# Optimization experiments

Measured on AMD Instinct MI355X. Metric: run time of the kernel, lower is better.

## Reference

```python
import jax, jax.numpy as jnp
import numpy as np

N = 50000      # nodes
E = 400000     # edges
D_IN = 128; D_HID = 128; D_OUT = 128
C = 8          # n_channel (== channel_dim)
CNF = 8        # channel_nf
DIM = 3        # spatial dim
EPS = 1e-3     # module eps
BN_EPS = 1e-5


def _pool_matrix(n_channel):
    # RollerPooling: pool_matrix[i] averages a sliding upper-triangular window of size (n-i)
    ones = np.ones((n_channel, n_channel), dtype=np.float32)
    mats = []
    for i in range(n_channel):
        w = n_channel - i
        mats.append((np.triu(ones) - np.triu(ones, k=w)) / w)
    return jnp.asarray(np.stack(mats))  # [C, C, C]


def setup_inputs() -> dict:
    key = jax.random.key(0)
    ks = jax.random.split(key, 20)
    s = 0.02
    src = jax.random.randint(ks[0], (E,), 0, N)
    tgt = jax.random.randint(ks[1], (E,), 0, N)
    rel = jnp.zeros((E,), dtype=src.dtype)  # num_relation = 1
    edge_list = jnp.stack([src, tgt, rel], axis=1)
    inp = {
        "h": jax.random.normal(ks[2], (N, D_IN), jnp.float32),
        "coords": jax.random.normal(ks[3], (N, C, DIM), jnp.float32),
        "channel_attr": jax.random.normal(ks[4], (N, C, CNF), jnp.float32),
        "channel_weights": jax.random.randint(ks[5], (N, C), 0, 3).astype(jnp.float32),
        "edge_weights": jax.random.uniform(ks[6], (E,), jnp.float32),
        "edge_list": edge_list,
        # parameters
        "rl_w": jax.random.normal(ks[7], (CNF * CNF, CNF), jnp.float32) * s,
        "rl_b": jnp.zeros((CNF,), jnp.float32),
        "m_w1": jax.random.normal(ks[8], (2 * D_IN + CNF, D_HID), jnp.float32) * s,
        "m_b1": jnp.zeros((D_HID,), jnp.float32),
        "m_w2": jax.random.normal(ks[9], (D_HID, D_HID), jnp.float32) * s,
        "m_b2": jnp.zeros((D_HID,), jnp.float32),
        "c_w1": jax.random.normal(ks[10], (D_HID, D_HID), jnp.float32) * s,
        "c_b1": jnp.zeros((D_HID,), jnp.float32),
        "c_w2": jax.random.normal(ks[11], (D_HID, C), jnp.float32) * 0.001,  # xavier gain=0.001
        "het_w": jax.random.normal(ks[12], (D_HID, D_OUT), jnp.float32) * s,
        "het_b": jnp.zeros((D_OUT,), jnp.float32),
        "bn_gamma": jnp.ones((D_OUT,), jnp.float32),
        "bn_beta": jnp.zeros((D_OUT,), jnp.float32),
        "w_r": jnp.ones((1,), jnp.float32),
    }
    return inp


def reference(h, coords, channel_attr, channel_weights, edge_weights,
              rl_w, rl_b, m_w1, m_b1, m_w2, m_b2, c_w1, c_b1, c_w2,
              het_w, het_b, bn_gamma, bn_beta, w_r, edge_list):
    silu = jax.nn.silu
    src, tgt, rel = edge_list[:, 0], edge_list[:, 1], edge_list[:, 2]
    n_channel = coords.shape[1]
    num_nodes = h.shape[0]

    # --- radial feature ---
    # pairwise channel distances per edge: [E, C, C]
    diff = coords[tgt][:, :, None, :] - coords[src][:, None, :, :]
    coord_msg = jnp.linalg.norm(diff, axis=-1)
    coord_msg = coord_msg / (jnp.max(coord_msg) + EPS)
    cw = channel_weights
    coord_msg = coord_msg * (cw[tgt][:, :, None] * cw[src][:, None, :])
    # attr_t^T @ msg @ attr_s -> [E, CNF, CNF]
    radial = jnp.einsum('eca,ecd,edb->eab', channel_attr[tgt], coord_msg, channel_attr[src])
    radial = radial.reshape(radial.shape[0], -1)
    radial = radial / (jnp.linalg.norm(radial, axis=-1, keepdims=True) + EPS)
    radial = radial @ rl_w + rl_b  # [E, CNF]

    mask = (cw != 0)
    csum = mask.sum(-1)  # [N]
    pooled_col = (coords[src] * mask[src][:, :, None].astype(coords.dtype)).sum(1)
    pooled_col = pooled_col / (csum[src][:, None].astype(coords.dtype) + EPS)
    coord_diff = coords[tgt] - pooled_col[:, None, :]  # [E, C, DIM]

    # --- message MLP (dropout = identity in eval) ---
    x = jnp.concatenate([h[tgt], h[src], radial], axis=-1)
    m = silu(x @ m_w1 + m_b1)
    m = silu(m @ m_w2 + m_b2)  # [E, hidden]

    # --- coord message with RollerPooling ---
    edge_feat = silu(m @ c_w1 + c_b1) @ c_w2  # [E, C]
    pm = _pool_matrix(n_channel)
    ts = jnp.clip(csum[tgt] - 1, 0, n_channel - 1)
    pooled_edge = jnp.einsum('eij,ej->ei', pm[ts], edge_feat)[..., None]  # [E, C, 1]
    coord_message = coord_diff * pooled_edge  # [E, C, DIM]

    # --- aggregate (scatter to target nodes) ---
    ew = edge_weights[:, None]
    node_agg = jax.ops.segment_sum(m * ew, tgt, num_segments=num_nodes)  # [N, hidden]
    wcm = w_r[rel][:, None, None] * coord_message
    coord_sum = jax.ops.segment_sum(wcm, tgt, num_segments=num_nodes)
    cnt = jax.ops.segment_sum(jnp.ones((wcm.shape[0],), wcm.dtype), tgt, num_segments=num_nodes)
    coord_agg = coord_sum / jnp.clip(cnt, 1.0)[:, None, None]  # mean aggregation

    # --- combine ---
    out = node_agg @ het_w + het_b
    # BatchNorm1d in eval mode with default running stats (mean=0, var=1)
    out = out / jnp.sqrt(1.0 + BN_EPS) * bn_gamma + bn_beta
    out = silu(out)
    node_output = h + out
    coord_output = coords + coord_agg
    return node_output, coord_output
```

## Files before the change

kernel.cpp:

```cpp
#include <hip/hip_runtime.h>

#define NN 50000
#define NE 400000
#define D 128
#define MST 136
#define EPSV 1e-3f

typedef unsigned short u16;
typedef unsigned int u32;
typedef __attribute__((ext_vector_type(4))) float f32x4;
typedef __attribute__((ext_vector_type(4))) float float4v;
typedef __attribute__((ext_vector_type(8))) short short8;
typedef __attribute__((ext_vector_type(8))) unsigned short ushort8;
typedef __attribute__((ext_vector_type(4))) unsigned short ushort4v;

__device__ __forceinline__ u16 f2b(float f){
  u32 u = __float_as_uint(f);
  u32 r = u + 0x7fffu + ((u >> 16) & 1u);
  return (u16)(r >> 16);
}
__device__ __forceinline__ float b2f(u16 s){ return __uint_as_float(((u32)s) << 16); }
__device__ __forceinline__ float silu_f(float x){
  return x * __builtin_amdgcn_rcpf(1.f + __expf(-x));
}
__device__ __forceinline__ void atomAddF(float* p, float v){ unsafeAtomicAdd(p, v); }

__global__ void k_prep_h(const float* __restrict__ h, u16* __restrict__ hbf){
  int i = (blockIdx.x * 256 + threadIdx.x) * 4;
  if (i < NN * D){
    float4v v = *(const float4v*)(h + i);
    ushort4v o = { f2b(v[0]), f2b(v[1]), f2b(v[2]), f2b(v[3]) };
    *(ushort4v*)(hbf + i) = o;
  }
}

__global__ void k_prep_w(const float* __restrict__ m_w1, const float* __restrict__ m_b1,
                         const float* __restrict__ m_w2, const float* __restrict__ c_w1,
                         const float* __restrict__ c_w2, const float* __restrict__ het_w,
                         u16* __restrict__ W12t, u16* __restrict__ W1cT,
                         u16* __restrict__ W2t, u16* __restrict__ C1t,
                         u16* __restrict__ HtT, u16* __restrict__ C2t){
  int i = blockIdx.x * 256 + threadIdx.x;
  if (i < 256 * 128){
    int c = i >> 7, k = i & 127;
    W12t[i] = f2b(c < 128 ? m_w1[k * D + c] : m_w1[(128 + k) * D + (c - 128)]);
    return;
  }
  i -= 256 * 128;
  if (i < 128 * 32){
    int c = i >> 5, j = i & 31;
    W1cT[i] = (j < 8) ? f2b(m_w1[(256 + j) * D + c]) : (j == 8 ? f2b(m_b1[c]) : (u16)0);
    return;
  }
  i -= 128 * 32;
  if (i < D * D){ int c = i >> 7, k = i & 127; W2t[i] = f2b(m_w2[k * D + c]); return; }
  i -= D * D;
  if (i < D * D){ int c = i >> 7, k = i & 127; C1t[i] = f2b(c_w1[k * D + c]); return; }
  i -= D * D;
  if (i < D * D){ int c = i >> 7, k = i & 127; HtT[i] = f2b(het_w[k * D + c]); return; }
  i -= D * D;
  if (i < 16 * D){ int n = i >> 7, k = i & 127; C2t[i] = f2b(n < 8 ? c_w2[k * 8 + n] : 0.f); return; }
}

__global__ void k_node_pre(const float* __restrict__ coords, const float* __restrict__ cw,
                           float* __restrict__ pooled, int* __restrict__ tsn){
  int n = blockIdx.x * 256 + threadIdx.x;
  if (n >= NN) return;
  int cs = 0; float px = 0.f, py = 0.f, pz = 0.f;
  #pragma unroll
  for (int c = 0; c < 8; c++){
    float w = cw[n * 8 + c];
    if (w != 0.f){
      cs++;
      px += coords[(size_t)n * 24 + c * 3 + 0];
      py += coords[(size_t)n * 24 + c * 3 + 1];
      pz += coords[(size_t)n * 24 + c * 3 + 2];
    }
  }
  float inv = 1.f / ((float)cs + EPSV);
  pooled[n * 3 + 0] = px * inv;
  pooled[n * 3 + 1] = py * inv;
  pooled[n * 3 + 2] = pz * inv;
  int ts = cs - 1; ts = ts < 0 ? 0 : (ts > 7 ? 7 : ts);
  tsn[n] = ts;
}

__global__ __launch_bounds__(256) void k_edge_max(const float* __restrict__ coords,
                                                  const int* __restrict__ el,
                                                  u32* __restrict__ maxsq, u32* __restrict__ cnt){
  int e = blockIdx.x * 256 + threadIdx.x;
  float vm = 0.f;
  if (e < NE){
    int s = el[e * 3 + 0], t = el[e * 3 + 1];
    float ct[24], cs_[24];
    const float4v* pt = (const float4v*)(coords + (size_t)t * 24);
    const float4v* ps = (const float4v*)(coords + (size_t)s * 24);
    #pragma unroll
    for (int i = 0; i < 6; i++){
      float4v v = pt[i];
      ct[i*4] = v[0]; ct[i*4+1] = v[1]; ct[i*4+2] = v[2]; ct[i*4+3] = v[3];
    }
    #pragma unroll
    for (int i = 0; i < 6; i++){
      float4v v = ps[i];
      cs_[i*4] = v[0]; cs_[i*4+1] = v[1]; cs_[i*4+2] = v[2]; cs_[i*4+3] = v[3];
    }
    #pragma unroll
    for (int c1 = 0; c1 < 8; c1++){
      #pragma unroll
      for (int c2 = 0; c2 < 8; c2++){
        float dx = ct[c1*3+0] - cs_[c2*3+0];
        float dy = ct[c1*3+1] - cs_[c2*3+1];
        float dz = ct[c1*3+2] - cs_[c2*3+2];
        vm = fmaxf(vm, dx*dx + dy*dy + dz*dz);
      }
    }
    atomicAdd(&cnt[t], 1u);
  }
  __shared__ float red[256];
  red[threadIdx.x] = vm;
  __syncthreads();
  for (int s2 = 128; s2 > 0; s2 >>= 1){
    if (threadIdx.x < s2) red[threadIdx.x] = fmaxf(red[threadIdx.x], red[threadIdx.x + s2]);
    __syncthreads();
  }
  if (threadIdx.x == 0) atomicMax(maxsq, __float_as_uint(red[0]));
}

__global__ __launch_bounds__(1024) void k_scan(const u32* __restrict__ cnt,
                                               u32* __restrict__ row_start,
                                               u32* __restrict__ fill_ptr){
  __shared__ u32 s[1024];
  const int tid = threadIdx.x;
  const int base = tid * 49;
  u32 tot = 0;
  #pragma unroll 1
  for (int k = 0; k < 49; k++){
    int i = base + k;
    if (i < NN) tot += cnt[i];
  }
  s[tid] = tot;
  __syncthreads();
  for (int off = 1; off < 1024; off <<= 1){
    u32 v = (tid >= off) ? s[tid - off] : 0u;
    __syncthreads();
    s[tid] += v;
    __syncthreads();
  }
  u32 running = s[tid] - tot;
  #pragma unroll 1
  for (int k = 0; k < 49; k++){
    int i = base + k;
    if (i <= NN){
      row_start[i] = running;
      if (i < NN){ fill_ptr[i] = running; running += cnt[i]; }
    }
  }
}

__global__ __launch_bounds__(256) void k_fill(const int* __restrict__ el,
                                              u32* __restrict__ fill_ptr,
                                              int* __restrict__ eidx){
  int e = blockIdx.x * 256 + threadIdx.x;
  if (e >= NE) return;
  int t = el[e * 3 + 1];
  u32 pos = atomicAdd(&fill_ptr[t], 1u);
  eidx[pos] = e;
}

__global__ __launch_bounds__(256) void k_radial(const float* __restrict__ coords,
                                                const float* __restrict__ attr,
                                                const float* __restrict__ cw,
                                                const int* __restrict__ el,
                                                const int* __restrict__ eidx,
                                                const float* __restrict__ ewg,
                                                const float* __restrict__ rl_w,
                                                const float* __restrict__ rl_b,
                                                const u32* __restrict__ maxsq,
                                                u16* __restrict__ rad8b,
                                                u32* __restrict__ st_s,
                                                float* __restrict__ ew_s){
  __shared__ float sct[64][24], scs[64][24], sAs[64][64], scwt[64][8], scws[64][8], stmp[64][64];
  const int tid = threadIdx.x;
  const int er = tid >> 2;
  const int q = tid & 3;
  const int p = blockIdx.x * 64 + er;
  const int e = eidx[p];
  const int s = el[e * 3 + 0];
  const int t = el[e * 3 + 1];
  if (q == 0){
    st_s[p] = ((u32)t << 16) | (u32)s;
    ew_s[p] = ewg[e];
  }

  #pragma unroll
  for (int i = 0; i < 6; i++) sct[er][q * 6 + i] = coords[(size_t)t * 24 + q * 6 + i];
  #pragma unroll
  for (int i = 0; i < 6; i++) scs[er][q * 6 + i] = coords[(size_t)s * 24 + q * 6 + i];
  #pragma unroll
  for (int i = 0; i < 16; i++) sAs[er][q * 16 + i] = attr[(size_t)s * 64 + q * 16 + i];
  #pragma unroll
  for (int i = 0; i < 2; i++){
    scwt[er][q * 2 + i] = cw[(size_t)t * 8 + q * 2 + i];
    scws[er][q * 2 + i] = cw[(size_t)s * 8 + q * 2 + i];
  }
  __syncthreads();

  const float scale = 1.f / (sqrtf(__uint_as_float(*maxsq)) + EPSV);

  float tmp[2][8];
  #pragma unroll
  for (int ci = 0; ci < 2; ci++)
    #pragma unroll
    for (int b = 0; b < 8; b++) tmp[ci][b] = 0.f;
  #pragma unroll
  for (int d = 0; d < 8; d++){
    float asd[8];
    #pragma unroll
    for (int b = 0; b < 8; b++) asd[b] = sAs[er][d * 8 + b];
    #pragma unroll
    for (int ci = 0; ci < 2; ci++){
      int c = q * 2 + ci;
      float dx = sct[er][c * 3 + 0] - scs[er][d * 3 + 0];
      float dy = sct[er][c * 3 + 1] - scs[er][d * 3 + 1];
      float dz = sct[er][c * 3 + 2] - scs[er][d * 3 + 2];
      float msg = sqrtf(dx * dx + dy * dy + dz * dz) * scale * scwt[er][c] * scws[er][d];
      #pragma unroll
      for (int b = 0; b < 8; b++) tmp[ci][b] += msg * asd[b];
    }
  }
  #pragma unroll
  for (int ci = 0; ci < 2; ci++)
    #pragma unroll
    for (int b = 0; b < 8; b++) stmp[er][(q * 2 + ci) * 8 + b] = tmp[ci][b];
  __syncthreads();

  float rad[2][8];
  #pragma unroll
  for (int ai = 0; ai < 2; ai++)
    #pragma unroll
    for (int b = 0; b < 8; b++) rad[ai][b] = 0.f;
  #pragma unroll
  for (int c = 0; c < 8; c++){
    float at0 = attr[(size_t)t * 64 + c * 8 + 2 * q + 0];
    float at1 = attr[(size_t)t * 64 + c * 8 + 2 * q + 1];
    #pragma unroll
    for (int b = 0; b < 8; b++){
      float tv = stmp[er][c * 8 + b];
      rad[0][b] += at0 * tv;
      rad[1][b] += at1 * tv;
    }
  }
  float sq = 0.f;
  #pragma unroll
  for (int ai = 0; ai < 2; ai++)
    #pragma unroll
    for (int b = 0; b < 8; b++) sq += rad[ai][b] * rad[ai][b];
  sq += __shfl_xor(sq, 1);
  sq += __shfl_xor(sq, 2);
  const float rn = 1.f / (sqrtf(sq) + EPSV);

  float o[8];
  #pragma unroll
  for (int j = 0; j < 8; j++) o[j] = 0.f;
  #pragma unroll
  for (int ai = 0; ai < 2; ai++){
    #pragma unroll
    for (int b = 0; b < 8; b++){
      float v = rad[ai][b] * rn;
      int row = (2 * q + ai) * 8 + b;
      #pragma unroll
      for (int j = 0; j < 8; j++) o[j] += v * rl_w[row * 8 + j];
    }
  }
  #pragma unroll
  for (int j = 0; j < 8; j++){
    o[j] += __shfl_xor(o[j], 1);
    o[j] += __shfl_xor(o[j], 2);
  }
  if (q == 0){
    ushort8 o8;
    #pragma unroll
    for (int j = 0; j < 8; j++) o8[j] = f2b(o[j] + rl_b[j]);
    *(ushort8*)(rad8b + (size_t)p * 8) = o8;
  }
}

__global__ __launch_bounds__(256) void k_hw12(const u16* __restrict__ hbf,
                                              const u16* __restrict__ W12t,
                                              float* __restrict__ hW12){
  __shared__ u16 sa[64 * MST];
  const int tid = threadIdx.x, lane = tid & 63, wv = tid >> 6, wrow = wv * 16;
  const int nb0 = blockIdx.x * 64;
  const int lc = lane & 15, lk = (lane >> 4) * 8;
  const f32x4 zero = {0.f, 0.f, 0.f, 0.f};

  #pragma unroll
  for (int jj = 0; jj < 4; jj++){
    const int flat = jj * 64 + lane;
    const int r = wrow + (flat >> 4);
    const int c8 = flat & 15;
    int rn = nb0 + r; if (rn >= NN) rn = NN - 1;
    *(ushort8*)(sa + r * MST + c8 * 8) = *(const ushort8*)(hbf + (size_t)rn * D + c8 * 8);
  }

  f32x4 acc[16];
  #pragma unroll
  for (int nb = 0; nb < 16; nb++) acc[nb] = zero;
  #pragma unroll
  for (int kb = 0; kb < 4; kb++){
    short8 a = *(const short8*)(sa + (wrow + lc) * MST + kb * 32 + lk);
    #pragma unroll
    for (int nb = 0; nb < 16; nb++){
      short8 b = *(const short8*)(W12t + (size_t)(nb * 16 + lc) * D + kb * 32 + lk);
      acc[nb] = __builtin_amdgcn_mfma_f32_16x16x32_bf16(a, b, acc[nb], 0, 0, 0);
    }
  }
  #pragma unroll
  for (int nb = 0; nb < 16; nb++){
    const int col = nb * 16 + lc;
    #pragma unroll
    for (int j = 0; j < 4; j++){
      const int row = wrow + (lane >> 4) * 4 + j;
      const int node = nb0 + row;
      if (node < NN) hW12[(size_t)node * 256 + col] = acc[nb][j];
    }
  }
}

__global__ __launch_bounds__(256, 2) void k_edge_mlp(
    const u16* __restrict__ rad8b, const u32* __restrict__ st_s,
    const float* __restrict__ ew_s, const float* __restrict__ hW12,
    const u16* __restrict__ W1cT, const u16* __restrict__ W2t,
    const u16* __restrict__ C1t, const u16* __restrict__ C2t,
    const float* __restrict__ m_b2, const float* __restrict__ c_b1,
    const int* __restrict__ tsn,
    float* __restrict__ out_node, float* __restrict__ pe8)
{
  __shared__ u16 sm[128 * MST];
  __shared__ float sef[128 * 8];
  __shared__ int s_tgt[128];
  __shared__ float s_ew[128];

  const int tid = threadIdx.x;
  const int lane = tid & 63;
  const int wv = tid >> 6;
  const int wr = wv * 32;
  const int e0 = blockIdx.x * 128;
  const int lc = lane & 15;
  const int khi = lane >> 4;
  const int lk = khi * 8;
  const f32x4 zero4 = {0.f, 0.f, 0.f, 0.f};
  const short8 zero8 = {0, 0, 0, 0, 0, 0, 0, 0};

  if (lane < 32){
    u32 v = st_s[e0 + wr + lane];
    s_tgt[wr + lane] = (int)(v >> 16);
    s_ew[wr + lane] = ew_s[e0 + wr + lane];
  }

  {
    const int r = wr + (lane >> 1);
    const int ch = (lane & 1) * 64;
    u32 v = st_s[e0 + r];
    const int t = (int)(v >> 16), s = (int)(v & 0xffffu);
    const float* pa = hW12 + (size_t)t * 256 + ch;
    const float* pb = hW12 + (size_t)s * 256 + 128 + ch;
    #pragma unroll
    for (int i = 0; i < 16; i++){
      float4v va = *(const float4v*)(pa + i * 4);
      float4v vb = *(const float4v*)(pb + i * 4);
      ushort4v o = { f2b(va[0] + vb[0]), f2b(va[1] + vb[1]),
                     f2b(va[2] + vb[2]), f2b(va[3] + vb[3]) };
      *(ushort4v*)(sm + r * MST + ch + i * 4) = o;
    }
  }

  f32x4 acc0[8], acc1[8];

  {
    short8 ar0, ar1;
    if (khi == 0){
      ar0 = *(const short8*)(rad8b + (size_t)(e0 + wr + lc) * 8);
      ar1 = *(const short8*)(rad8b + (size_t)(e0 + wr + 16 + lc) * 8);
    } else if (khi == 1){
      ar0 = zero8; ar0[0] = (short)0x3F80;
      ar1 = ar0;
    } else {
      ar0 = zero8; ar1 = zero8;
    }
    #pragma unroll
    for (int nb = 0; nb < 8; nb++){
      short8 b = *(const short8*)(W1cT + (size_t)(nb * 16 + lc) * 32 + lk);
      acc0[nb] = __builtin_amdgcn_mfma_f32_16x16x32_bf16(ar0, b, zero4, 0, 0, 0);
      acc1[nb] = __builtin_amdgcn_mfma_f32_16x16x32_bf16(ar1, b, zero4, 0, 0, 0);
    }
  }
  #pragma unroll
  for (int nb = 0; nb < 8; nb++){
    const int col = nb * 16 + lc;
    #pragma unroll
    for (int j = 0; j < 4; j++){
      const int r0 = wr + khi * 4 + j;
      const int r1 = r0 + 16;
      float v0 = silu_f(acc0[nb][j] + b2f(sm[r0 * MST + col]));
      float v1 = silu_f(acc1[nb][j] + b2f(sm[r1 * MST + col]));
      sm[r0 * MST + col] = f2b(v0);
// ... 81 lines not shown
      short8 a1 = *(const short8*)(sm + (wr + 16 + lc) * MST + kb * 32 + lk);
      short8 b = *(const short8*)(C2t + (size_t)lc * D + kb * 32 + lk);
      e40 = __builtin_amdgcn_mfma_f32_16x16x32_bf16(a0, b, e40, 0, 0, 0);
      e41 = __builtin_amdgcn_mfma_f32_16x16x32_bf16(a1, b, e41, 0, 0, 0);
    }
    if (lc < 8){
      #pragma unroll
      for (int j = 0; j < 4; j++){
        sef[(wr + khi * 4 + j) * 8 + lc] = e40[j];
        sef[(wr + 16 + khi * 4 + j) * 8 + lc] = e41[j];
      }
    }
  }

  {
    const int er = wr + (lane >> 1);
    const int q4 = (lane & 1) * 4;
    const int t = s_tgt[er];
    const int w8 = 8 - tsn[t];
    const float invw = 1.f / (float)w8;
    float4v o;
    #pragma unroll
    for (int ci = 0; ci < 4; ci++){
      const int c = q4 + ci;
      float pe = 0.f;
      const int hi = (c + w8 < 8) ? (c + w8) : 8;
      for (int j = c; j < hi; j++) pe += sef[er * 8 + j];
      o[ci] = pe * invw;
    }
    *(float4v*)(pe8 + (size_t)(e0 + er) * 8 + q4) = o;
  }
}

__global__ __launch_bounds__(256) void k_agg(
    const u32* __restrict__ row_start, const float* __restrict__ pe8,
    const u32* __restrict__ st_s, const float* __restrict__ pooled,
    const float* __restrict__ coords, const float* __restrict__ w_r,
    float* __restrict__ out_coord)
{
  const int lane = threadIdx.x & 63;
  const int wv = threadIdx.x >> 6;
  const int n = blockIdx.x * 4 + wv;
  if (n >= NN) return;
  const u32 r0 = row_start[n], r1 = row_start[n + 1];
  const int cA = lane / 3, dA = lane - cA * 3;
  float sp = 0.f, sqd = 0.f;
  for (u32 p = r0; p < r1; p++){
    if (lane < 8)  sp  += pe8[(size_t)p * 8 + lane];
    if (lane < 24) sqd += pooled[(size_t)(st_s[p] & 0xffffu) * 3 + dA] * pe8[(size_t)p * 8 + cA];
  }
  if (lane < 24){
    const float wr0 = w_r[0];
    const float spc = __shfl(sp, cA);
    const float cv = coords[(size_t)n * 24 + lane];
    const u32 deg = r1 - r0;
    const float dv = (float)(deg > 0u ? deg : 1u);
    out_coord[(size_t)n * 24 + lane] = cv + wr0 * (cv * spc - sqd) / dv;
  }
}

__global__ __launch_bounds__(256) void k_final(
    const float* __restrict__ h, const u16* __restrict__ HtT,
    const float* __restrict__ het_b, const float* __restrict__ bn_g,
    const float* __restrict__ bn_b, float* __restrict__ out_node)
{
  __shared__ u16 sa[64 * MST];
  const int tid = threadIdx.x, lane = tid & 63, wv = tid >> 6, wrow = wv * 16;
  const int nb0 = blockIdx.x * 64;
  const int lc = lane & 15, lk = (lane >> 4) * 8;
  const f32x4 zero = {0.f, 0.f, 0.f, 0.f};

  #pragma unroll
  for (int jj = 0; jj < 8; jj++){
    const int idx = jj * 64 + lane;
    const int r = wrow + (idx >> 5);
    const int c4 = (idx & 31) * 4;
    int rn = nb0 + r; if (rn >= NN) rn = NN - 1;
    float4v v = *(const float4v*)(out_node + (size_t)rn * D + c4);
    ushort4v o = { f2b(v[0]), f2b(v[1]), f2b(v[2]), f2b(v[3]) };
    *(ushort4v*)(sa + r * MST + c4) = o;
  }

  f32x4 acc[8];
  #pragma unroll
  for (int nb = 0; nb < 8; nb++) acc[nb] = zero;
  #pragma unroll
  for (int kb = 0; kb < 4; kb++){
    short8 a = *(const short8*)(sa + (wrow + lc) * MST + kb * 32 + lk);
    #pragma unroll
    for (int nb = 0; nb < 8; nb++){
      short8 b = *(const short8*)(HtT + (size_t)(nb * 16 + lc) * D + kb * 32 + lk);
      acc[nb] = __builtin_amdgcn_mfma_f32_16x16x32_bf16(a, b, acc[nb], 0, 0, 0);
    }
  }
  const float invs = rsqrtf(1.f + 1e-5f);
  #pragma unroll
  for (int nb = 0; nb < 8; nb++){
    const int col = nb * 16 + lc;
    const float hb = het_b[col], g = bn_g[col], be = bn_b[col];
    #pragma unroll
    for (int j = 0; j < 4; j++){
      const int row = wrow + (lane >> 4) * 4 + j;
      const int node = nb0 + row;
      if (node < NN){
        float v = silu_f((acc[nb][j] + hb) * invs * g + be);
        out_node[(size_t)node * D + col] = v + h[(size_t)node * D + col];
      }
    }
  }
}

extern "C" void kernel_launch(void* const* d_in, const int* in_sizes, int n_in,
                              void* d_out, int out_size, void* d_ws, size_t ws_size,
                              hipStream_t stream)
{
  const float* h      = (const float*)d_in[0];
  const float* coords = (const float*)d_in[1];
  const float* cattr  = (const float*)d_in[2];
  const float* cw     = (const float*)d_in[3];
  const float* ewg    = (const float*)d_in[4];
  const int*   el     = (const int*)  d_in[5];
  const float* rl_w   = (const float*)d_in[6];
  const float* rl_b   = (const float*)d_in[7];
  const float* m_w1   = (const float*)d_in[8];
  const float* m_b1   = (const float*)d_in[9];
  const float* m_w2   = (const float*)d_in[10];
  const float* m_b2   = (const float*)d_in[11];
  const float* c_w1   = (const float*)d_in[12];
  const float* c_b1   = (const float*)d_in[13];
  const float* c_w2   = (const float*)d_in[14];
  const float* het_w  = (const float*)d_in[15];
  const float* het_b  = (const float*)d_in[16];
  const float* bn_g   = (const float*)d_in[17];
  const float* bn_b   = (const float*)d_in[18];
  const float* w_r    = (const float*)d_in[19];

  char* wsb = (char*)d_ws;
  size_t off = 0;
  auto take = [&](size_t bytes)->char*{
    char* p = wsb + off;
    off = (off + bytes + 255) & ~(size_t)255;
    return p;
  };
  u32*   maxsq  = (u32*)  take(4);
  float* pooled = (float*)take((size_t)NN * 3 * 4);
  int*   tsn    = (int*)  take((size_t)NN * 4);
  u32*   cnt    = (u32*)  take((size_t)NN * 4);
  u16*   hbf    = (u16*)  take((size_t)NN * D * 2);
  u16*   W12t   = (u16*)  take((size_t)256 * D * 2);
  u16*   W1cT   = (u16*)  take((size_t)D * 32 * 2);
  u16*   W2t    = (u16*)  take((size_t)D * D * 2);
  u16*   C1t    = (u16*)  take((size_t)D * D * 2);
  u16*   HtT    = (u16*)  take((size_t)D * D * 2);
  u16*   C2t    = (u16*)  take((size_t)16 * D * 2);
  u32*   row_start = (u32*)  take((size_t)(NN + 1) * 4);
  u32*   fill_ptr  = (u32*)  take((size_t)NN * 4);
  int*   eidx      = (int*)  take((size_t)NE * 4);
  u32*   st_s      = (u32*)  take((size_t)NE * 4);
  float* ew_s      = (float*)take((size_t)NE * 4);
  u16*   rad8b     = (u16*)  take((size_t)NE * 8 * 2);
  float* pe8       = (float*)take((size_t)NE * 8 * 4);
  float* hW12      = (float*)take((size_t)NN * 256 * 4);
  (void)ws_size;

  float* out_node  = (float*)d_out;
  float* out_coord = out_node + (size_t)NN * D;

  (void)hipMemsetAsync(maxsq, 0, 4, stream);
  (void)hipMemsetAsync(cnt, 0, (size_t)NN * 4, stream);
  (void)hipMemsetAsync(out_node, 0, (size_t)NN * D * 4, stream);

  k_prep_h  <<<dim3((NN * D / 4 + 255) / 256), dim3(256), 0, stream>>>(h, hbf);
  k_prep_w  <<<dim3((256*128 + 128*32 + 3*D*D + 16*D + 255) / 256), dim3(256), 0, stream>>>(
        m_w1, m_b1, m_w2, c_w1, c_w2, het_w, W12t, W1cT, W2t, C1t, HtT, C2t);
  k_node_pre<<<dim3((NN + 255) / 256), dim3(256), 0, stream>>>(coords, cw, pooled, tsn);
  k_edge_max<<<dim3((NE + 255) / 256), dim3(256), 0, stream>>>(coords, el, maxsq, cnt);
  k_scan    <<<dim3(1), dim3(1024), 0, stream>>>(cnt, row_start, fill_ptr);
  k_fill    <<<dim3((NE + 255) / 256), dim3(256), 0, stream>>>(el, fill_ptr, eidx);
  k_radial  <<<dim3(NE / 64), dim3(256), 0, stream>>>(
        coords, cattr, cw, el, eidx, ewg, rl_w, rl_b, maxsq, rad8b, st_s, ew_s);
  k_hw12    <<<dim3((NN + 63) / 64), dim3(256), 0, stream>>>(hbf, W12t, hW12);
  k_edge_mlp<<<dim3(NE / 128), dim3(256), 0, stream>>>(
        rad8b, st_s, ew_s, hW12, W1cT, W2t, C1t, C2t, m_b2, c_b1, tsn, out_node, pe8);
  k_agg     <<<dim3((NN + 3) / 4), dim3(256), 0, stream>>>(
        row_start, pe8, st_s, pooled, coords, w_r, out_coord);
  k_final   <<<dim3((NN + 63) / 64), dim3(256), 0, stream>>>(
        h, HtT, het_b, bn_g, bn_b, out_node);
}
```

Before: 784.0 us.

## Merge independent kernels into block-partitioned launches and store hW12 as bf16

Independent stages now share launches: the prep kernels become one, radial plus hW12 become one, and agg plus final become one, with blocks dispatched by block-index ranges. This cuts launch count and lets the independent work in each launch run side by side. The radial kernel now works from registers with two lanes per edge instead of staging through shared memory. The hW12 intermediate is stored as bf16 instead of fp32, halving its gather traffic in the edge MLP at some cost in precision. The two memsets are also merged into one by placing maxsq right after cnt.

```diff
diff --git a/kernel.cpp b/kernel.cpp
--- a/kernel.cpp
+++ b/kernel.cpp
@@ -25,106 +25,120 @@
 }
 __device__ __forceinline__ void atomAddF(float* p, float v){ unsafeAtomicAdd(p, v); }
 
-__global__ void k_prep_h(const float* __restrict__ h, u16* __restrict__ hbf){
-  int i = (blockIdx.x * 256 + threadIdx.x) * 4;
-  if (i < NN * D){
-    float4v v = *(const float4v*)(h + i);
-    ushort4v o = { f2b(v[0]), f2b(v[1]), f2b(v[2]), f2b(v[3]) };
-    *(ushort4v*)(hbf + i) = o;
-  }
-}
-
-__global__ void k_prep_w(const float* __restrict__ m_w1, const float* __restrict__ m_b1,
-                         const float* __restrict__ m_w2, const float* __restrict__ c_w1,
-                         const float* __restrict__ c_w2, const float* __restrict__ het_w,
-                         u16* __restrict__ W12t, u16* __restrict__ W1cT,
-                         u16* __restrict__ W2t, u16* __restrict__ C1t,
-                         u16* __restrict__ HtT, u16* __restrict__ C2t){
-  int i = blockIdx.x * 256 + threadIdx.x;
-  if (i < 256 * 128){
-    int c = i >> 7, k = i & 127;
-    W12t[i] = f2b(c < 128 ? m_w1[k * D + c] : m_w1[(128 + k) * D + (c - 128)]);
+#define PH_B 6250
+#define PW_B 344
+#define NP_B 196
+#define EM_B 1563
+__global__ __launch_bounds__(256) void K0_prep(
+    const float* __restrict__ h, const float* __restrict__ coords,
+    const float* __restrict__ cw, const int* __restrict__ el,
+    const float* __restrict__ m_w1, const float* __restrict__ m_b1,
+    const float* __restrict__ m_w2, const float* __restrict__ c_w1,
+    const float* __restrict__ c_w2, const float* __restrict__ het_w,
+    u16* __restrict__ hbf, u16* __restrict__ W12t, u16* __restrict__ W1cT,
+    u16* __restrict__ W2t, u16* __restrict__ C1t, u16* __restrict__ HtT,
+    u16* __restrict__ C2t, float* __restrict__ pooled, int* __restrict__ tsn,
+    u32* __restrict__ maxsq, u32* __restrict__ cnt)
+{
+  __shared__ float red[256];
+  int bid = blockIdx.x;
+  const int tid = threadIdx.x;
+
+  if (bid < PH_B){
+    int i = (bid * 256 + tid) * 4;
+    if (i < NN * D){
+      float4v v = *(const float4v*)(h + i);
+      ushort4v o = { f2b(v[0]), f2b(v[1]), f2b(v[2]), f2b(v[3]) };
+      *(ushort4v*)(hbf + i) = o;
+    }
     return;
   }
-  i -= 256 * 128;
-  if (i < 128 * 32){
-    int c = i >> 5, j = i & 31;
-    W1cT[i] = (j < 8) ? f2b(m_w1[(256 + j) * D + c]) : (j == 8 ? f2b(m_b1[c]) : (u16)0);
+  bid -= PH_B;
+  if (bid < PW_B){
+    int i = bid * 256 + tid;
+    if (i < 256 * 128){
+      int c = i >> 7, k = i & 127;
+      W12t[i] = f2b(c < 128 ? m_w1[k * D + c] : m_w1[(128 + k) * D + (c - 128)]);
+      return;
+    }
+    i -= 256 * 128;
+    if (i < 128 * 32){
+      int c = i >> 5, j = i & 31;
+      W1cT[i] = (j < 8) ? f2b(m_w1[(256 + j) * D + c]) : (j == 8 ? f2b(m_b1[c]) : (u16)0);
+      return;
+    }
+    i -= 128 * 32;
+    if (i < D * D){ int c = i >> 7, k = i & 127; W2t[i] = f2b(m_w2[k * D + c]); return; }
+    i -= D * D;
+    if (i < D * D){ int c = i >> 7, k = i & 127; C1t[i] = f2b(c_w1[k * D + c]); return; }
+    i -= D * D;
+    if (i < D * D){ int c = i >> 7, k = i & 127; HtT[i] = f2b(het_w[k * D + c]); return; }
+    i -= D * D;
+    if (i < 16 * D){ int n = i >> 7, k = i & 127; C2t[i] = f2b(n < 8 ? c_w2[k * 8 + n] : 0.f); }
     return;
   }
-  i -= 128 * 32;
-  if (i < D * D){ int c = i >> 7, k = i & 127; W2t[i] = f2b(m_w2[k * D + c]); return; }
-  i -= D * D;
-  if (i < D * D){ int c = i >> 7, k = i & 127; C1t[i] = f2b(c_w1[k * D + c]); return; }
-  i -= D * D;
-  if (i < D * D){ int c = i >> 7, k = i & 127; HtT[i] = f2b(het_w[k * D + c]); return; }
-  i -= D * D;
-  if (i < 16 * D){ int n = i >> 7, k = i & 127; C2t[i] = f2b(n < 8 ? c_w2[k * 8 + n] : 0.f); return; }
-}
-
-__global__ void k_node_pre(const float* __restrict__ coords, const float* __restrict__ cw,
-                           float* __restrict__ pooled, int* __restrict__ tsn){
-  int n = blockIdx.x * 256 + threadIdx.x;
-  if (n >= NN) return;
-  int cs = 0; float px = 0.f, py = 0.f, pz = 0.f;
-  #pragma unroll
-  for (int c = 0; c < 8; c++){
-    float w = cw[n * 8 + c];
-    if (w != 0.f){
-      cs++;
-      px += coords[(size_t)n * 24 + c * 3 + 0];
-      py += coords[(size_t)n * 24 + c * 3 + 1];
-      pz += coords[(size_t)n * 24 + c * 3 + 2];
-    }
-  }
-  float inv = 1.f / ((float)cs + EPSV);
-  pooled[n * 3 + 0] = px * inv;
-  pooled[n * 3 + 1] = py * inv;
-  pooled[n * 3 + 2] = pz * inv;
-  int ts = cs - 1; ts = ts < 0 ? 0 : (ts > 7 ? 7 : ts);
-  tsn[n] = ts;
-}
-
-__global__ __launch_bounds__(256) void k_edge_max(const float* __restrict__ coords,
-                                                  const int* __restrict__ el,
-                                                  u32* __restrict__ maxsq, u32* __restrict__ cnt){
-  int e = blockIdx.x * 256 + threadIdx.x;
-  float vm = 0.f;
-  if (e < NE){
-    int s = el[e * 3 + 0], t = el[e * 3 + 1];
-    float ct[24], cs_[24];
-    const float4v* pt = (const float4v*)(coords + (size_t)t * 24);
-    const float4v* ps = (const float4v*)(coords + (size_t)s * 24);
-    #pragma unroll
-    for (int i = 0; i < 6; i++){
-      float4v v = pt[i];
-      ct[i*4] = v[0]; ct[i*4+1] = v[1]; ct[i*4+2] = v[2]; ct[i*4+3] = v[3];
-    }
-    #pragma unroll
-    for (int i = 0; i < 6; i++){
-      float4v v = ps[i];
-      cs_[i*4] = v[0]; cs_[i*4+1] = v[1]; cs_[i*4+2] = v[2]; cs_[i*4+3] = v[3];
-    }
-    #pragma unroll
-    for (int c1 = 0; c1 < 8; c1++){
-      #pragma unroll
-      for (int c2 = 0; c2 < 8; c2++){
-        float dx = ct[c1*3+0] - cs_[c2*3+0];
-        float dy = ct[c1*3+1] - cs_[c2*3+1];
-        float dz = ct[c1*3+2] - cs_[c2*3+2];
-        vm = fmaxf(vm, dx*dx + dy*dy + dz*dz);
-      }
-    }
-    atomicAdd(&cnt[t], 1u);
-  }
-  __shared__ float red[256];
-  red[threadIdx.x] = vm;
-  __syncthreads();
-  for (int s2 = 128; s2 > 0; s2 >>= 1){
-    if (threadIdx.x < s2) red[threadIdx.x] = fmaxf(red[threadIdx.x], red[threadIdx.x + s2]);
+  bid -= PW_B;
+  if (bid < NP_B){
+    int n = bid * 256 + tid;
+    if (n >= NN) return;
+    int cs = 0; float px = 0.f, py = 0.f, pz = 0.f;
+    #pragma unroll
+    for (int c = 0; c < 8; c++){
+      float w = cw[n * 8 + c];
+      if (w != 0.f){
+        cs++;
+        px += coords[(size_t)n * 24 + c * 3 + 0];
+        py += coords[(size_t)n * 24 + c * 3 + 1];
+        pz += coords[(size_t)n * 24 + c * 3 + 2];
+      }
+    }
+    float inv = 1.f / ((float)cs + EPSV);
+    pooled[n * 3 + 0] = px * inv;
+    pooled[n * 3 + 1] = py * inv;
+    pooled[n * 3 + 2] = pz * inv;
+    int ts = cs - 1; ts = ts < 0 ? 0 : (ts > 7 ? 7 : ts);
+    tsn[n] = ts;
+    return;
+  }
+  bid -= NP_B;
+  {
+    int e = bid * 256 + tid;
+    float vm = 0.f;
+    if (e < NE){
+      int s = el[e * 3 + 0], t = el[e * 3 + 1];
+      float ct[24], cs_[24];
+      const float4v* pt = (const float4v*)(coords + (size_t)t * 24);
+      const float4v* ps = (const float4v*)(coords + (size_t)s * 24);
+      #pragma unroll
+      for (int i = 0; i < 6; i++){
+        float4v v = pt[i];
+        ct[i*4] = v[0]; ct[i*4+1] = v[1]; ct[i*4+2] = v[2]; ct[i*4+3] = v[3];
+      }
+      #pragma unroll
+      for (int i = 0; i < 6; i++){
+        float4v v = ps[i];
+        cs_[i*4] = v[0]; cs_[i*4+1] = v[1]; cs_[i*4+2] = v[2]; cs_[i*4+3] = v[3];
+      }
+      #pragma unroll
+      for (int c1 = 0; c1 < 8; c1++){
+        #pragma unroll
+        for (int c2 = 0; c2 < 8; c2++){
+          float dx = ct[c1*3+0] - cs_[c2*3+0];
+          float dy = ct[c1*3+1] - cs_[c2*3+1];
+          float dz = ct[c1*3+2] - cs_[c2*3+2];
+          vm = fmaxf(vm, dx*dx + dy*dy + dz*dz);
+        }
+      }
+      atomicAdd(&cnt[t], 1u);
+    }
+    red[tid] = vm;
     __syncthreads();
-  }
-  if (threadIdx.x == 0) atomicMax(maxsq, __float_as_uint(red[0]));
+    for (int s2 = 128; s2 > 0; s2 >>= 1){
+      if (tid < s2) red[tid] = fmaxf(red[tid], red[tid + s2]);
+      __syncthreads();
+    }
+    if (tid == 0) atomicMax(maxsq, __float_as_uint(red[0]));
+  }
 }
 
 __global__ __launch_bounds__(1024) void k_scan(const u32* __restrict__ cnt,
@@ -168,169 +182,193 @@
   eidx[pos] = e;
 }
 
-__global__ __launch_bounds__(256) void k_radial(const float* __restrict__ coords,
-                                                const float* __restrict__ attr,
-                                                const float* __restrict__ cw,
-                                                const int* __restrict__ el,
-                                                const int* __restrict__ eidx,
-                                                const float* __restrict__ ewg,
-                                                const float* __restrict__ rl_w,
-                                                const float* __restrict__ rl_b,
-                                                const u32* __restrict__ maxsq,
-                                                u16* __restrict__ rad8b,
-                                                u32* __restrict__ st_s,
-                                                float* __restrict__ ew_s){
-  __shared__ float sct[64][24], scs[64][24], sAs[64][64], scwt[64][8], scws[64][8], stmp[64][64];
+#define RAD_B 3125
+#define HW_B 782
+__global__ __launch_bounds__(256) void K3_radial_hw12(
+    const float* __restrict__ coords, const float* __restrict__ attr,
+    const float* __restrict__ cw, const int* __restrict__ el,
+    const int* __restrict__ eidx, const float* __restrict__ ewg,
+    const float* __restrict__ rl_w, const float* __restrict__ rl_b,
+    const u32* __restrict__ maxsq,
+    const u16* __restrict__ hbf, const u16* __restrict__ W12t,
+    u16* __restrict__ rad8b, u32* __restrict__ st_s, float* __restrict__ ew_s,
+    u16* __restrict__ hW12b)
+{
+  __shared__ u16 sa[64 * MST];
+  __shared__ float srl[64 * 8 + 8];
   const int tid = threadIdx.x;
-  const int er = tid >> 2;
-  const int q = tid & 3;
-  const int p = blockIdx.x * 64 + er;
-  const int e = eidx[p];
-  const int s = el[e * 3 + 0];
-  const int t = el[e * 3 + 1];
-  if (q == 0){
-    st_s[p] = ((u32)t << 16) | (u32)s;
-    ew_s[p] = ewg[e];
-  }
-
-  #pragma unroll
-  for (int i = 0; i < 6; i++) sct[er][q * 6 + i] = coords[(size_t)t * 24 + q * 6 + i];
-  #pragma unroll
-  for (int i = 0; i < 6; i++) scs[er][q * 6 + i] = coords[(size_t)s * 24 + q * 6 + i];
-  #pragma unroll
-  for (int i = 0; i < 16; i++) sAs[er][q * 16 + i] = attr[(size_t)s * 64 + q * 16 + i];
-  #pragma unroll
-  for (int i = 0; i < 2; i++){
-    scwt[er][q * 2 + i] = cw[(size_t)t * 8 + q * 2 + i];
-    scws[er][q * 2 + i] = cw[(size_t)s * 8 + q * 2 + i];
-  }
-  __syncthreads();
-
-  const float scale = 1.f / (sqrtf(__uint_as_float(*maxsq)) + EPSV);
-
-  float tmp[2][8];
-  #pragma unroll
-  for (int ci = 0; ci < 2; ci++)
-    #pragma unroll
-    for (int b = 0; b < 8; b++) tmp[ci][b] = 0.f;
-  #pragma unroll
-  for (int d = 0; d < 8; d++){
-    float asd[8];
-    #pragma unroll
-    for (int b = 0; b < 8; b++) asd[b] = sAs[er][d * 8 + b];
-    #pragma unroll
-    for (int ci = 0; ci < 2; ci++){
-      int c = q * 2 + ci;
-      float dx = sct[er][c * 3 + 0] - scs[er][d * 3 + 0];
-      float dy = sct[er][c * 3 + 1] - scs[er][d * 3 + 1];
-      float dz = sct[er][c * 3 + 2] - scs[er][d * 3 + 2];
-      float msg = sqrtf(dx * dx + dy * dy + dz * dz) * scale * scwt[er][c] * scws[er][d];
-      #pragma unroll
-      for (int b = 0; b < 8; b++) tmp[ci][b] += msg * asd[b];
-    }
-  }
-  #pragma unroll
-  for (int ci = 0; ci < 2; ci++)
-    #pragma unroll
-    for (int b = 0; b < 8; b++) stmp[er][(q * 2 + ci) * 8 + b] = tmp[ci][b];
-  __syncthreads();
-
-  float rad[2][8];
-  #pragma unroll
-  for (int ai = 0; ai < 2; ai++)
-    #pragma unroll
-    for (int b = 0; b < 8; b++) rad[ai][b] = 0.f;
-  #pragma unroll
-  for (int c = 0; c < 8; c++){
-    float at0 = attr[(size_t)t * 64 + c * 8 + 2 * q + 0];
-    float at1 = attr[(size_t)t * 64 + c * 8 + 2 * q + 1];
-    #pragma unroll
-    for (int b = 0; b < 8; b++){
-      float tv = stmp[er][c * 8 + b];
-      rad[0][b] += at0 * tv;
-      rad[1][b] += at1 * tv;
-    }
-  }
-  float sq = 0.f;
-  #pragma unroll
-  for (int ai = 0; ai < 2; ai++)
-    #pragma unroll
-    for (int b = 0; b < 8; b++) sq += rad[ai][b] * rad[ai][b];
-  sq += __shfl_xor(sq, 1);
-  sq += __shfl_xor(sq, 2);
-  const float rn = 1.f / (sqrtf(sq) + EPSV);
-
-  float o[8];
-  #pragma unroll
-  for (int j = 0; j < 8; j++) o[j] = 0.f;
-  #pragma unroll
-  for (int ai = 0; ai < 2; ai++){
-    #pragma unroll
-    for (int b = 0; b < 8; b++){
-      float v = rad[ai][b] * rn;
-      int row = (2 * q + ai) * 8 + b;
-      #pragma unroll
-      for (int j = 0; j < 8; j++) o[j] += v * rl_w[row * 8 + j];
-    }
-  }
-  #pragma unroll
-  for (int j = 0; j < 8; j++){
-    o[j] += __shfl_xor(o[j], 1);
-    o[j] += __shfl_xor(o[j], 2);
-  }
-  if (q == 0){
-    ushort8 o8;
-    #pragma unroll
-    for (int j = 0; j < 8; j++) o8[j] = f2b(o[j] + rl_b[j]);
-    *(ushort8*)(rad8b + (size_t)p * 8) = o8;
-  }
-}
-
-__global__ __launch_bounds__(256) void k_hw12(const u16* __restrict__ hbf,
-                                              const u16* __restrict__ W12t,
-                                              float* __restrict__ hW12){
-  __shared__ u16 sa[64 * MST];
-  const int tid = threadIdx.x, lane = tid & 63, wv = tid >> 6, wrow = wv * 16;
-  const int nb0 = blockIdx.x * 64;
-  const int lc = lane & 15, lk = (lane >> 4) * 8;
-  const f32x4 zero = {0.f, 0.f, 0.f, 0.f};
-
-  #pragma unroll
-  for (int jj = 0; jj < 4; jj++){
-    const int flat = jj * 64 + lane;
-    const int r = wrow + (flat >> 4);
-    const int c8 = flat & 15;
-    int rn = nb0 + r; if (rn >= NN) rn = NN - 1;
-    *(ushort8*)(sa + r * MST + c8 * 8) = *(const ushort8*)(hbf + (size_t)rn * D + c8 * 8);
-  }
-
-  f32x4 acc[16];
-  #pragma unroll
-  for (int nb = 0; nb < 16; nb++) acc[nb] = zero;
-  #pragma unroll
-  for (int kb = 0; kb < 4; kb++){
-    short8 a = *(const short8*)(sa + (wrow + lc) * MST + kb * 32 + lk);
+  int bid = blockIdx.x;
+
+  if (bid < RAD_B){
+    {
+      float v = (tid < 512) ? rl_w[tid] : (tid < 520 ? rl_b[tid - 512] : 0.f);
+      if (tid < 520) srl[tid] = v;
+    }
+    __syncthreads();
+
+    const int lane = tid & 63;
+    const int wv = tid >> 6;
+    const int eh = lane >> 1;
+    const int q = lane & 1;
+    const int p = bid * 128 + wv * 32 + eh;
+    const int e = eidx[p];
+    const int s = el[e * 3 + 0];
+    const int t = el[e * 3 + 1];
+    if (q == 0){
+      st_s[p] = ((u32)t << 16) | (u32)s;
+      ew_s[p] = ewg[e];
+    }
+
+    float ct[12], cs_[24], cwt[4], cws[8];
+    {
+      const float* pt = coords + (size_t)t * 24 + q * 12;
+      #pragma unroll
+      for (int i = 0; i < 3; i++){
+        float4v v = *(const float4v*)(pt + i * 4);
+        ct[i*4] = v[0]; ct[i*4+1] = v[1]; ct[i*4+2] = v[2]; ct[i*4+3] = v[3];
+      }
+      const float* ps = coords + (size_t)s * 24;
+      #pragma unroll
+      for (int i = 0; i < 6; i++){
+        float4v v = *(const float4v*)(ps + i * 4);
+        cs_[i*4] = v[0]; cs_[i*4+1] = v[1]; cs_[i*4+2] = v[2]; cs_[i*4+3] = v[3];
+      }
+      float4v vt = *(const float4v*)(cw + (size_t)t * 8 + q * 4);
+      cwt[0] = vt[0]; cwt[1] = vt[1]; cwt[2] = vt[2]; cwt[3] = vt[3];
+      float4v v0 = *(const float4v*)(cw + (size_t)s * 8);
+      float4v v1 = *(const float4v*)(cw + (size_t)s * 8 + 4);
+      cws[0]=v0[0]; cws[1]=v0[1]; cws[2]=v0[2]; cws[3]=v0[3];
+      cws[4]=v1[0]; cws[5]=v1[1]; cws[6]=v1[2]; cws[7]=v1[3];
+    }
+    const float scale = 1.f / (sqrtf(__uint_as_float(*maxsq)) + EPSV);
+
+    float tmp[4][8];
+    #pragma unroll
+    for (int ci = 0; ci < 4; ci++)
+      #pragma unroll
+      for (int b = 0; b < 8; b++) tmp[ci][b] = 0.f;
+    #pragma unroll
+    for (int d = 0; d < 8; d++){
+      float asd[8];
+      {
+        const float* pa = attr + (size_t)s * 64 + d * 8;
+        float4v a0 = *(const float4v*)(pa);
+        float4v a1 = *(const float4v*)(pa + 4);
+        asd[0]=a0[0]; asd[1]=a0[1]; asd[2]=a0[2]; asd[3]=a0[3];
+        asd[4]=a1[0]; asd[5]=a1[1]; asd[6]=a1[2]; asd[7]=a1[3];
+      }
+      const float csd0 = cs_[d*3+0], csd1 = cs_[d*3+1], csd2 = cs_[d*3+2];
+      const float cwsd = cws[d] * scale;
+      #pragma unroll
+      for (int ci = 0; ci < 4; ci++){
+        float dx = ct[ci*3+0] - csd0;
+        float dy = ct[ci*3+1] - csd1;
+        float dz = ct[ci*3+2] - csd2;
+        float msg = sqrtf(dx*dx + dy*dy + dz*dz) * cwsd * cwt[ci];
+        #pragma unroll
+        for (int b = 0; b < 8; b++) tmp[ci][b] += msg * asd[b];
+      }
+    }
+
+    float rad[8][8];
+    #pragma unroll
+    for (int a = 0; a < 8; a++)
+      #pragma unroll
+      for (int b = 0; b < 8; b++) rad[a][b] = 0.f;
+    #pragma unroll
+    for (int ci = 0; ci < 4; ci++){
+      const int c = q * 4 + ci;
+      float atc[8];
+      const float* pa = attr + (size_t)t * 64 + c * 8;
+      float4v a0 = *(const float4v*)(pa);
+      float4v a1 = *(const float4v*)(pa + 4);
+      atc[0]=a0[0]; atc[1]=a0[1]; atc[2]=a0[2]; atc[3]=a0[3];
+      atc[4]=a1[0]; atc[5]=a1[1]; atc[6]=a1[2]; atc[7]=a1[3];
+      #pragma unroll
+      for (int a = 0; a < 8; a++)
+        #pragma unroll
+        for (int b = 0; b < 8; b++) rad[a][b] += atc[a] * tmp[ci][b];
+    }
+    #pragma unroll
+    for (int a = 0; a < 8; a++)
+      #pragma unroll
+      for (int b = 0; b < 8; b++) rad[a][b] += __shfl_xor(rad[a][b], 1);
+
+    float sq = 0.f;
+    #pragma unroll
+    for (int a = 0; a < 8; a++)
+      #pragma unroll
+      for (int b = 0; b < 8; b++) sq += rad[a][b] * rad[a][b];
+    const float rn = 1.f / (sqrtf(sq) + EPSV);
+
+    float o[8];
+    #pragma unroll
+    for (int j = 0; j < 8; j++) o[j] = 0.f;
+    #pragma unroll
+    for (int ai = 0; ai < 4; ai++){
+      const int a = q * 4 + ai;
+      #pragma unroll
+      for (int b = 0; b < 8; b++){
+        const float v = rad[a][b] * rn;
+        const int row = a * 8 + b;
+        #pragma unroll
+        for (int j = 0; j < 8; j++) o[j] += v * srl[row * 8 + j];
+      }
+    }
+    #pragma unroll
+    for (int j = 0; j < 8; j++) o[j] += __shfl_xor(o[j], 1);
+    if (q == 0){
+      ushort8 o8;
+      #pragma unroll
+      for (int j = 0; j < 8; j++) o8[j] = f2b(o[j] + srl[512 + j]);
+      *(ushort8*)(rad8b + (size_t)p * 8) = o8;
+    }
+    return;
+  }
+  bid -= RAD_B;
+  {
+    const int lane = tid & 63, wv = tid >> 6, wrow = wv * 16;
+    const int nb0 = bid * 64;
+    const int lc = lane & 15, lk = (lane >> 4) * 8;
+    const f32x4 zero = {0.f, 0.f, 0.f, 0.f};
+
+    #pragma unroll
+    for (int jj = 0; jj < 4; jj++){
+      const int flat = jj * 64 + lane;
+      const int r = wrow + (flat >> 4);
+      const int c8 = flat & 15;
+      int rn2 = nb0 + r; if (rn2 >= NN) rn2 = NN - 1;
+      *(ushort8*)(sa + r * MST + c8 * 8) = *(const ushort8*)(hbf + (size_t)rn2 * D + c8 * 8);
+    }
+
+    f32x4 acc[16];
+    #pragma unroll
+    for (int nb = 0; nb < 16; nb++) acc[nb] = zero;
+    #pragma unroll
+    for (int kb = 0; kb < 4; kb++){
+      short8 a = *(const short8*)(sa + (wrow + lc) * MST + kb * 32 + lk);
+      #pragma unroll
+      for (int nb = 0; nb < 16; nb++){
+        short8 b = *(const short8*)(W12t + (size_t)(nb * 16 + lc) * D + kb * 32 + lk);
+        acc[nb] = __builtin_amdgcn_mfma_f32_16x16x32_bf16(a, b, acc[nb], 0, 0, 0);
+      }
+    }
     #pragma unroll
     for (int nb = 0; nb < 16; nb++){
-      short8 b = *(const short8*)(W12t + (size_t)(nb * 16 + lc) * D + kb * 32 + lk);
-      acc[nb] = __builtin_amdgcn_mfma_f32_16x16x32_bf16(a, b, acc[nb], 0, 0, 0);
-    }
-  }
-  #pragma unroll
-  for (int nb = 0; nb < 16; nb++){
-    const int col = nb * 16 + lc;
-    #pragma unroll
-    for (int j = 0; j < 4; j++){
-      const int row = wrow + (lane >> 4) * 4 + j;
-      const int node = nb0 + row;
-      if (node < NN) hW12[(size_t)node * 256 + col] = acc[nb][j];
-    }
-  }
-}
-
-__global__ __launch_bounds__(256, 2) void k_edge_mlp(
+      const int col = nb * 16 + lc;
+      #pragma unroll
+      for (int j = 0; j < 4; j++){
+        const int row = wrow + (lane >> 4) * 4 + j;
+        const int node = nb0 + row;
+        if (node < NN) hW12b[(size_t)node * 256 + col] = f2b(acc[nb][j]);
+      }
+    }
+  }
+}
+
+__global__ __launch_bounds__(256, 4) void k_edge_mlp(
     const u16* __restrict__ rad8b, const u32* __restrict__ st_s,
-    const float* __restrict__ ew_s, const float* __restrict__ hW12,
+    const float* __restrict__ ew_s, const u16* __restrict__ hW12b,
     const u16* __restrict__ W1cT, const u16* __restrict__ W2t,
     const u16* __restrict__ C1t, const u16* __restrict__ C2t,
     const float* __restrict__ m_b2, const float* __restrict__ c_b1,
@@ -364,15 +402,16 @@
     const int ch = (lane & 1) * 64;
     u32 v = st_s[e0 + r];
     const int t = (int)(v >> 16), s = (int)(v & 0xffffu);
-    const float* pa = hW12 + (size_t)t * 256 + ch;
-    const float* pb = hW12 + (size_t)s * 256 + 128 + ch;
-    #pragma unroll
-    for (int i = 0; i < 16; i++){
-      float4v va = *(const float4v*)(pa + i * 4);
-      float4v vb = *(const float4v*)(pb + i * 4);
-      ushort4v o = { f2b(va[0] + vb[0]), f2b(va[1] + vb[1]),
-                     f2b(va[2] + vb[2]), f2b(va[3] + vb[3]) };
-      *(ushort4v*)(sm + r * MST + ch + i * 4) = o;
+    const u16* pa = hW12b + (size_t)t * 256 + ch;
+    const u16* pb = hW12b + (size_t)s * 256 + 128 + ch;
+    #pragma unroll
+    for (int i = 0; i < 8; i++){
+      ushort8 va = *(const ushort8*)(pa + i * 8);
+      ushort8 vb = *(const ushort8*)(pb + i * 8);
+      ushort8 o;
+      #pragma unroll
+      for (int j = 0; j < 8; j++) o[j] = f2b(b2f((u16)va[j]) + b2f((u16)vb[j]));
+      *(ushort8*)(sm + r * MST + ch + i * 8) = o;
     }
   }
 
@@ -520,79 +559,86 @@
   }
 }
 
-__global__ __launch_bounds__(256) void k_agg(
+#define AGG_B 12500
+#define FIN_B 782
+__global__ __launch_bounds__(256) void K5_agg_final(
     const u32* __restrict__ row_start, const float* __restrict__ pe8,
     const u32* __restrict__ st_s, const float* __restrict__ pooled,
     const float* __restrict__ coords, const float* __restrict__ w_r,
-    float* __restrict__ out_coord)
-{
-  const int lane = threadIdx.x & 63;
-  const int wv = threadIdx.x >> 6;
-  const int n = blockIdx.x * 4 + wv;
-  if (n >= NN) return;
-  const u32 r0 = row_start[n], r1 = row_start[n + 1];
-  const int cA = lane / 3, dA = lane - cA * 3;
-  float sp = 0.f, sqd = 0.f;
-  for (u32 p = r0; p < r1; p++){
-    if (lane < 8)  sp  += pe8[(size_t)p * 8 + lane];
-    if (lane < 24) sqd += pooled[(size_t)(st_s[p] & 0xffffu) * 3 + dA] * pe8[(size_t)p * 8 + cA];
-  }
-  if (lane < 24){
-    const float wr0 = w_r[0];
-    const float spc = __shfl(sp, cA);
-    const float cv = coords[(size_t)n * 24 + lane];
-    const u32 deg = r1 - r0;
-    const float dv = (float)(deg > 0u ? deg : 1u);
-    out_coord[(size_t)n * 24 + lane] = cv + wr0 * (cv * spc - sqd) / dv;
-  }
-}
-
-__global__ __launch_bounds__(256) void k_final(
     const float* __restrict__ h, const u16* __restrict__ HtT,
     const float* __restrict__ het_b, const float* __restrict__ bn_g,
-    const float* __restrict__ bn_b, float* __restrict__ out_node)
+    const float* __restrict__ bn_b,
+    float* __restrict__ out_node, float* __restrict__ out_coord)
 {
   __shared__ u16 sa[64 * MST];
-  const int tid = threadIdx.x, lane = tid & 63, wv = tid >> 6, wrow = wv * 16;
-  const int nb0 = blockIdx.x * 64;
-  const int lc = lane & 15, lk = (lane >> 4) * 8;
-  const f32x4 zero = {0.f, 0.f, 0.f, 0.f};
-
-  #pragma unroll
-  for (int jj = 0; jj < 8; jj++){
-    const int idx = jj * 64 + lane;
-    const int r = wrow + (idx >> 5);
-    const int c4 = (idx & 31) * 4;
-    int rn = nb0 + r; if (rn >= NN) rn = NN - 1;
-    float4v v = *(const float4v*)(out_node + (size_t)rn * D + c4);
-    ushort4v o = { f2b(v[0]), f2b(v[1]), f2b(v[2]), f2b(v[3]) };
-    *(ushort4v*)(sa + r * MST + c4) = o;
-  }
-
-  f32x4 acc[8];
-  #pragma unroll
-  for (int nb = 0; nb < 8; nb++) acc[nb] = zero;
-  #pragma unroll
-  for (int kb = 0; kb < 4; kb++){
-    short8 a = *(const short8*)(sa + (wrow + lc) * MST + kb * 32 + lk);
+  const int tid = threadIdx.x;
+  int bid = blockIdx.x;
+
+  if (bid < AGG_B){
+    const int lane = tid & 63;
+    const int wv = tid >> 6;
+    const int n = bid * 4 + wv;
+    if (n >= NN) return;
+    const u32 r0 = row_start[n], r1 = row_start[n + 1];
+    const int cA = lane / 3, dA = lane - cA * 3;
+    float sp = 0.f, sqd = 0.f;
+    for (u32 p = r0; p < r1; p++){
+      if (lane < 8)  sp  += pe8[(size_t)p * 8 + lane];
+      if (lane < 24) sqd += pooled[(size_t)(st_s[p] & 0xffffu) * 3 + dA] * pe8[(size_t)p * 8 + cA];
+    }
+    if (lane < 24){
+      const float wr0 = w_r[0];
+      const float spc = __shfl(sp, cA);
+      const float cv = coords[(size_t)n * 24 + lane];
+      const u32 deg = r1 - r0;
+      const float dv = (float)(deg > 0u ? deg : 1u);
+      out_coord[(size_t)n * 24 + lane] = cv + wr0 * (cv * spc - sqd) / dv;
+    }
+    return;
+  }
+  bid -= AGG_B;
+  {
+    const int lane = tid & 63, wv = tid >> 6, wrow = wv * 16;
+    const int nb0 = bid * 64;
+    const int lc = lane & 15, lk = (lane >> 4) * 8;
+    const f32x4 zero = {0.f, 0.f, 0.f, 0.f};
+
+    #pragma unroll
+    for (int jj = 0; jj < 8; jj++){
+      const int idx = jj * 64 + lane;
+      const int r = wrow + (idx >> 5);
+      const int c4 = (idx & 31) * 4;
+      int rn = nb0 + r; if (rn >= NN) rn = NN - 1;
+      float4v v = *(const float4v*)(out_node + (size_t)rn * D + c4);
+      ushort4v o = { f2b(v[0]), f2b(v[1]), f2b(v[2]), f2b(v[3]) };
+      *(ushort4v*)(sa + r * MST + c4) = o;
+    }
+
+    f32x4 acc[8];
+    #pragma unroll
+    for (int nb = 0; nb < 8; nb++) acc[nb] = zero;
+    #pragma unroll
+    for (int kb = 0; kb < 4; kb++){
+      short8 a = *(const short8*)(sa + (wrow + lc) * MST + kb * 32 + lk);
+      #pragma unroll
+      for (int nb = 0; nb < 8; nb++){
+        short8 b = *(const short8*)(HtT + (size_t)(nb * 16 + lc) * D + kb * 32 + lk);
+        acc[nb] = __builtin_amdgcn_mfma_f32_16x16x32_bf16(a, b, acc[nb], 0, 0, 0);
+      }
+    }
+    const float invs = rsqrtf(1.f + 1e-5f);
     #pragma unroll
     for (int nb = 0; nb < 8; nb++){
-      short8 b = *(const short8*)(HtT + (size_t)(nb * 16 + lc) * D + kb * 32 + lk);
-      acc[nb] = __builtin_amdgcn_mfma_f32_16x16x32_bf16(a, b, acc[nb], 0, 0, 0);
-    }
-  }
-  const float invs = rsqrtf(1.f + 1e-5f);
-  #pragma unroll
-  for (int nb = 0; nb < 8; nb++){
-    const int col = nb * 16 + lc;
-    const float hb = het_b[col], g = bn_g[col], be = bn_b[col];
-    #pragma unroll
-    for (int j = 0; j < 4; j++){
-      const int row = wrow + (lane >> 4) * 4 + j;
-      const int node = nb0 + row;
-      if (node < NN){
-        float v = silu_f((acc[nb][j] + hb) * invs * g + be);
-        out_node[(size_t)node * D + col] = v + h[(size_t)node * D + col];
+      const int col = nb * 16 + lc;
+      const float hb = het_b[col], g = bn_g[col], be = bn_b[col];
+      #pragma unroll
+      for (int j = 0; j < 4; j++){
+        const int row = wrow + (lane >> 4) * 4 + j;
+        const int node = nb0 + row;
+        if (node < NN){
+          float v = silu_f((acc[nb][j] + hb) * invs * g + be);
+          out_node[(size_t)node * D + col] = v + h[(size_t)node * D + col];
+        }
       }
     }
   }
@@ -630,10 +676,10 @@
     off = (off + bytes + 255) & ~(size_t)255;
     return p;
   };
-  u32*   maxsq  = (u32*)  take(4);
+  u32*   cnt    = (u32*)  take((size_t)(NN + 1) * 4);
+  u32*   maxsq  = cnt + NN;
   float* pooled = (float*)take((size_t)NN * 3 * 4);
   int*   tsn    = (int*)  take((size_t)NN * 4);
-  u32*   cnt    = (u32*)  take((size_t)NN * 4);
   u16*   hbf    = (u16*)  take((size_t)NN * D * 2);
   u16*   W12t   = (u16*)  take((size_t)256 * D * 2);
   u16*   W1cT   = (u16*)  take((size_t)D * 32 * 2);
@@ -648,30 +694,26 @@
   float* ew_s      = (float*)take((size_t)NE * 4);
   u16*   rad8b     = (u16*)  take((size_t)NE * 8 * 2);
   float* pe8       = (float*)take((size_t)NE * 8 * 4);
-  float* hW12      = (float*)take((size_t)NN * 256 * 4);
+  u16*   hW12b     = (u16*)  take((size_t)NN * 256 * 2);
   (void)ws_size;
 
   float* out_node  = (float*)d_out;
   float* out_coord = out_node + (size_t)NN * D;
 
-  (void)hipMemsetAsync(maxsq, 0, 4, stream);
-  (void)hipMemsetAsync(cnt, 0, (size_t)NN * 4, stream);
+  (void)hipMemsetAsync(cnt, 0, (size_t)(NN + 1) * 4, stream);
   (void)hipMemsetAsync(out_node, 0, (size_t)NN * D * 4, stream);
 
-  k_prep_h  <<<dim3((NN * D / 4 + 255) / 256), dim3(256), 0, stream>>>(h, hbf);
-  k_prep_w  <<<dim3((256*128 + 128*32 + 3*D*D + 16*D + 255) / 256), dim3(256), 0, stream>>>(
-        m_w1, m_b1, m_w2, c_w1, c_w2, het_w, W12t, W1cT, W2t, C1t, HtT, C2t);
-  k_node_pre<<<dim3((NN + 255) / 256), dim3(256), 0, stream>>>(coords, cw, pooled, tsn);
-  k_edge_max<<<dim3((NE + 255) / 256), dim3(256), 0, stream>>>(coords, el, maxsq, cnt);
-  k_scan    <<<dim3(1), dim3(1024), 0, stream>>>(cnt, row_start, fill_ptr);
-  k_fill    <<<dim3((NE + 255) / 256), dim3(256), 0, stream>>>(el, fill_ptr, eidx);
-  k_radial  <<<dim3(NE / 64), dim3(256), 0, stream>>>(
-        coords, cattr, cw, el, eidx, ewg, rl_w, rl_b, maxsq, rad8b, st_s, ew_s);
-  k_hw12    <<<dim3((NN + 63) / 64), dim3(256), 0, stream>>>(hbf, W12t, hW12);
+  K0_prep<<<dim3(PH_B + PW_B + NP_B + EM_B), dim3(256), 0, stream>>>(
+      h, coords, cw, el, m_w1, m_b1, m_w2, c_w1, c_w2, het_w,
+      hbf, W12t, W1cT, W2t, C1t, HtT, C2t, pooled, tsn, maxsq, cnt);
+  k_scan<<<dim3(1), dim3(1024), 0, stream>>>(cnt, row_start, fill_ptr);
+  k_fill<<<dim3((NE + 255) / 256), dim3(256), 0, stream>>>(el, fill_ptr, eidx);
+  K3_radial_hw12<<<dim3(RAD_B + HW_B), dim3(256), 0, stream>>>(
+      coords, cattr, cw, el, eidx, ewg, rl_w, rl_b, maxsq,
+      hbf, W12t, rad8b, st_s, ew_s, hW12b);
   k_edge_mlp<<<dim3(NE / 128), dim3(256), 0, stream>>>(
-        rad8b, st_s, ew_s, hW12, W1cT, W2t, C1t, C2t, m_b2, c_b1, tsn, out_node, pe8);
-  k_agg     <<<dim3((NN + 3) / 4), dim3(256), 0, stream>>>(
-        row_start, pe8, st_s, pooled, coords, w_r, out_coord);
-  k_final   <<<dim3((NN + 63) / 64), dim3(256), 0, stream>>>(
-        h, HtT, het_b, bn_g, bn_b, out_node);
-}
+      rad8b, st_s, ew_s, hW12b, W1cT, W2t, C1t, C2t, m_b2, c_b1, tsn, out_node, pe8);
+  K5_agg_final<<<dim3(AGG_B + FIN_B), dim3(256), 0, stream>>>(
+      row_start, pe8, st_s, pooled, coords, w_r,
+      h, HtT, het_b, bn_g, bn_b, out_node, out_coord);
+}
```

After: 727.4 us. 1.08x faster.
